# Optimization experiments

Hardware: AMD Instinct MI355X
Metric: run time of the kernel (lower is better)

Reference implementation:

```python
import jax, jax.numpy as jnp
import numpy as np

D_MODEL = 1024
NUM_HEADS = 16
HEAD_DIM = D_MODEL // NUM_HEADS


def setup_inputs() -> dict:
    key = jax.random.key(0)
    ks = jax.random.split(key, 5)
    scale = 1.0 / np.sqrt(D_MODEL)
    x = jax.random.normal(ks[0], (2, 2048, D_MODEL), dtype=jnp.float32)
    W_qkv = jax.random.normal(ks[1], (D_MODEL, 3 * D_MODEL), dtype=jnp.float32) * scale
    b_qkv = jnp.zeros((3 * D_MODEL,), dtype=jnp.float32)
    W_proj = jax.random.normal(ks[2], (D_MODEL, D_MODEL), dtype=jnp.float32) * scale
    b_proj = jnp.zeros((D_MODEL,), dtype=jnp.float32)
    return {"x": x, "W_qkv": W_qkv, "b_qkv": b_qkv, "W_proj": W_proj, "b_proj": b_proj}


def reference(x, W_qkv, b_qkv, W_proj, b_proj):
    B, S, D = x.shape
    qkv = x @ W_qkv + b_qkv                      # [B,S,3D]
    qkv = qkv.reshape(B, S, 3, NUM_HEADS, HEAD_DIM)
    qkv = jnp.transpose(qkv, (2, 0, 3, 1, 4))    # [3,B,H,S,hd]
    q, k, v = qkv[0], qkv[1], qkv[2]
    scores = jnp.einsum('bhqd,bhkd->bhqk', q, k) / jnp.sqrt(jnp.asarray(HEAD_DIM, x.dtype))
    probs = jax.nn.softmax(scores, axis=-1)
    out = jnp.einsum('bhqk,bhkd->bhqd', probs, v)  # [B,H,S,hd]
    out = jnp.transpose(out, (0, 2, 1, 3)).reshape(B, S, D)
    return out @ W_proj + b_proj
```

## Files before the change

### kernel.cpp

```cpp
#include <hip/hip_runtime.h>
#include <math.h>

#define B_ 2
#define S_ 2048
#define D_ 1024
#define H_ 16
#define HD_ 64

typedef __bf16 bf16x8 __attribute__((ext_vector_type(8)));
typedef __bf16 bf16x4 __attribute__((ext_vector_type(4)));
typedef __bf16 bf16x2 __attribute__((ext_vector_type(2)));
typedef float f32x4 __attribute__((ext_vector_type(4)));
typedef float f32x16 __attribute__((ext_vector_type(16)));
typedef unsigned u32x2 __attribute__((ext_vector_type(2)));

#define GLOAD16(gsrc, ldst) \
  __builtin_amdgcn_global_load_lds((const __attribute__((address_space(1))) void*)(gsrc), \
                                   (__attribute__((address_space(3))) void*)(ldst), 16, 0, 0)

#define QSCALE 0.18033688f

static __device__ __forceinline__ unsigned pack2(float a, float b) {
    bf16x2 v; v[0] = (__bf16)a; v[1] = (__bf16)b;
    return __builtin_bit_cast(unsigned, v);
}

__global__ __launch_bounds__(256) void prep_k(
    const float* __restrict__ x, __bf16* __restrict__ x_bf,
    const float* __restrict__ Wqkv, __bf16* __restrict__ wq_t,
    const float* __restrict__ Wproj, __bf16* __restrict__ wp_t)
{
    __shared__ float t[64][65];
    const int tid = threadIdx.x;
    const int bid = blockIdx.x;

    if (bid < 2048) {
        int i = (bid * 256 + tid) * 8;
        float4 a = *(const float4*)(x + i);
        float4 b = *(const float4*)(x + i + 4);
        bf16x8 v;
        v[0] = (__bf16)a.x; v[1] = (__bf16)a.y; v[2] = (__bf16)a.z; v[3] = (__bf16)a.w;
        v[4] = (__bf16)b.x; v[5] = (__bf16)b.y; v[6] = (__bf16)b.z; v[7] = (__bf16)b.w;
        *(bf16x8*)(x_bf + i) = v;
        return;
    }

    const float* in; __bf16* outp; int K, N, qcols; float qs; int bx, by;
    if (bid < 2816) {
        int tt = bid - 2048; bx = tt % 48; by = tt / 48;
        in = Wqkv; outp = wq_t; K = D_; N = 3 * D_; qcols = D_; qs = QSCALE;
    } else {
        int tt = bid - 2816; bx = tt % 16; by = tt / 16;
        in = Wproj; outp = wp_t; K = D_; N = D_; qcols = 0; qs = 1.0f;
    }
    const int bj = bx * 64;
    const int bi = by * 64;
    #pragma unroll
    for (int it = 0; it < 4; ++it) {
        int idx = (tid + it * 256) * 4;
        int r = idx >> 6, c = idx & 63;
        float4 v = *(const float4*)(in + (size_t)(bi + r) * N + bj + c);
        t[r][c] = v.x; t[r][c+1] = v.y; t[r][c+2] = v.z; t[r][c+3] = v.w;
    }
    __syncthreads();
    int j = tid & 63;
    int i0 = (tid >> 6) * 16;
    float s = (bj + j) < qcols ? qs : 1.0f;
    bf16x8 h0, h1;
    #pragma unroll
    for (int ii = 0; ii < 8; ++ii) h0[ii] = (__bf16)(t[i0 + ii][j] * s);
    #pragma unroll
    for (int ii = 0; ii < 8; ++ii) h1[ii] = (__bf16)(t[i0 + 8 + ii][j] * s);
    size_t o = (size_t)(bj + j) * K + bi + i0;
    *(bf16x8*)(outp + o) = h0; *(bf16x8*)(outp + o + 8) = h1;
}

template<typename OutT>
__global__ __launch_bounds__(256) void gemm_nt_k(
    const __bf16* __restrict__ A, const __bf16* __restrict__ Bt,
    const float* __restrict__ bias, OutT* __restrict__ C,
    int M, int N, int K, int qcols, float qs)
{
    constexpr int TSZ = 128 * 64;
    __shared__ __bf16 sA[TSZ];
    __shared__ __bf16 sB[TSZ];

    const int tid = threadIdx.x, w = tid >> 6, l = tid & 63;
    const int lr = l & 15, lg = l >> 4;
    const int bm = blockIdx.y * 128, bn = blockIdx.x * 128;
    const int wm = w >> 1, wn = w & 1;

    f32x4 acc[4][4] = {};

    for (int k0 = 0; k0 < K; k0 += 64) {
        __syncthreads();
        #pragma unroll
        for (int c = 0; c < 4; ++c) {
            int q = w * 4 + c;
            int r = q * 8 + (l >> 3);
            int sl = ((l & 7) ^ (r & 7)) * 8;
            GLOAD16(A + (size_t)(bm + r) * K + k0 + sl, sA + q * 512);
            GLOAD16(Bt + (size_t)(bn + r) * K + k0 + sl, sB + q * 512);
        }
        __syncthreads();
        #pragma unroll
        for (int kk = 0; kk < 2; ++kk) {
            bf16x8 ah[4], bh[4];
            #pragma unroll
            for (int i = 0; i < 4; ++i) {
                int ra = wm * 64 + i * 16 + lr;
                int sa = ((kk * 4 + lg) ^ (ra & 7)) * 8;
                ah[i] = *(const bf16x8*)(sA + ra * 64 + sa);
                int rb = wn * 64 + i * 16 + lr;
                int sb = ((kk * 4 + lg) ^ (rb & 7)) * 8;
                bh[i] = *(const bf16x8*)(sB + rb * 64 + sb);
            }
            #pragma unroll
            for (int mi = 0; mi < 4; ++mi)
                #pragma unroll
                for (int ni = 0; ni < 4; ++ni)
                    acc[mi][ni] = __builtin_amdgcn_mfma_f32_16x16x32_bf16(ah[mi], bh[ni], acc[mi][ni], 0, 0, 0);
        }
    }

    #pragma unroll
    for (int ni = 0; ni < 4; ++ni) {
        int col = bn + wn * 64 + ni * 16 + lr;
        float bv = bias[col];
        if (col < qcols) bv *= qs;
        #pragma unroll
        for (int mi = 0; mi < 4; ++mi) {
            #pragma unroll
            for (int r = 0; r < 4; ++r) {
                int row = bm + wm * 64 + mi * 16 + lg * 4 + r;
                float v = acc[mi][ni][r] + bv;
                C[(size_t)row * N + col] = (OutT)v;
            }
        }
    }
}

__global__ __launch_bounds__(256, 2) void attn32_k(
    const __bf16* __restrict__ qkv, __bf16* __restrict__ Pout,
    float* __restrict__ Lout)
{
    __shared__ __bf16 Ks[2][64 * 64];
    __shared__ __bf16 Vt[2][64 * 64];

    const int tid = threadIdx.x, w = tid >> 6, l = tid & 63;
    const int q32 = l & 31, hi = l >> 5;
    const int bid = blockIdx.x;
    const int X = bid >> 5, hb = bid & 31;
    const int qt = X >> 1, kvh = X & 1;
    const int h = hb >> 1, b = hb & 1;
    const int q0 = qt * 256;
    const int kvbase = kvh * 1024;
    const size_t ldq = 3 * D_;
    const __bf16* Qg = qkv + (size_t)b * S_ * ldq + h * HD_;
    const __bf16* Kg = Qg + D_;
    const __bf16* Vg = Qg + 2 * D_;
    const int qg0 = q0 + w * 64 + q32;

    bf16x8 qf0[4], qf1[4];
    #pragma unroll
    for (int ds = 0; ds < 4; ++ds) {
        qf0[ds] = *(const bf16x8*)(Qg + (size_t)qg0 * ldq + ds * 16 + hi * 8);
        qf1[ds] = *(const bf16x8*)(Qg + (size_t)(qg0 + 32) * ldq + ds * 16 + hi * 8);
    }

    int krow[2], ksl[2], voff[2][8];
    const int vk = l;
    #pragma unroll
    for (int c = 0; c < 2; ++c) {
        int p = (w * 2 + c) * 64 + l;
        krow[c] = p >> 3;
        ksl[c]  = (p & 7) ^ (krow[c] & 7);
        int d0 = (w * 2 + c) * 8;
        #pragma unroll
        for (int j = 0; j < 8; ++j)
            voff[c][j] = (d0 + j) * 128 + (((vk >> 3) ^ j) * 16) + (vk & 7) * 2;
    }

    f32x16 o0[2] = {}, o1[2] = {};
    float lsum0 = 0.f, lsum1 = 0.f;
    bf16x8 vr[2];

    auto stageK = [&](int lt, int buf) {
        #pragma unroll
        for (int c = 0; c < 2; ++c)
            GLOAD16(Kg + (size_t)(kvbase + lt * 64 + krow[c]) * ldq + ksl[c] * 8,
                    &Ks[buf][(w * 2 + c) * 512]);
    };
    auto loadV = [&](int lt) {
        #pragma unroll
        for (int c = 0; c < 2; ++c)
            vr[c] = *(const bf16x8*)(Vg + (size_t)(kvbase + lt * 64 + vk) * ldq + (w * 2 + c) * 8);
    };
    auto writeV = [&](int buf) {
        #pragma unroll
        for (int c = 0; c < 2; ++c)
            #pragma unroll
            for (int j = 0; j < 8; ++j)
                *(__bf16*)((char*)&Vt[buf][0] + voff[c][j]) = vr[c][j];
    };

    auto smPack = [&](f32x16 sc[2], bf16x8 pa[2][2], float& ls) {
        float sum = 0.f;
        #pragma unroll
        for (int kb = 0; kb < 2; ++kb)
            #pragma unroll
            for (int i = 0; i < 16; ++i) {
                float pv = __builtin_amdgcn_exp2f(sc[kb][i]);
                sc[kb][i] = pv;
                sum += pv;
            }
        ls += sum;
        #pragma unroll
        for (int kb = 0; kb < 2; ++kb)
            #pragma unroll
            for (int tl = 0; tl < 2; ++tl) {
                int base = tl * 8;
                unsigned A0 = pack2(sc[kb][base + 0], sc[kb][base + 1]);
                unsigned A1 = pack2(sc[kb][base + 2], sc[kb][base + 3]);
                unsigned B0 = pack2(sc[kb][base + 4], sc[kb][base + 5]);
                unsigned B1 = pack2(sc[kb][base + 6], sc[kb][base + 7]);
                u32x2 s0 = __builtin_amdgcn_permlane32_swap(A0, B0, false, false);
                u32x2 s1 = __builtin_amdgcn_permlane32_swap(A1, B1, false, false);
                union { unsigned u[4]; bf16x8 v; } pu;
                pu.u[0] = s0[0]; pu.u[1] = s1[0]; pu.u[2] = s0[1]; pu.u[3] = s1[1];
                pa[kb][tl] = pu.v;
            }
    };

    auto computeTile = [&](int cur) {
        f32x16 sc0[2] = {}, sc1[2] = {};
        __builtin_amdgcn_s_setprio(1);
        #pragma unroll
        for (int kb = 0; kb < 2; ++kb) {
            int r = kb * 32 + q32;
            #pragma unroll
            for (int ds = 0; ds < 4; ++ds) {
                int slot = (ds * 2 + hi) ^ (r & 7);
                bf16x8 kf = *(const bf16x8*)((const char*)&Ks[cur][0] + r * 128 + slot * 16);
                sc0[kb] = __builtin_amdgcn_mfma_f32_32x32x16_bf16(kf, qf0[ds], sc0[kb], 0, 0, 0);
                sc1[kb] = __builtin_amdgcn_mfma_f32_32x32x16_bf16(kf, qf1[ds], sc1[kb], 0, 0, 0);
            }
        }
        __builtin_amdgcn_s_setprio(0);

        bf16x8 pa0[2][2], pa1[2][2];
        smPack(sc0, pa0, lsum0);
        smPack(sc1, pa1, lsum1);

        __builtin_amdgcn_s_setprio(1);
        #pragma unroll
        for (int db = 0; db < 2; ++db) {
            int dr = db * 32 + q32;
            #pragma unroll
            for (int tt = 0; tt < 4; ++tt) {
                int slot = (tt * 2 + hi) ^ (dr & 7);
                bf16x8 vf = *(const bf16x8*)((const char*)&Vt[cur][0] + dr * 128 + slot * 16);
                o0[db] = __builtin_amdgcn_mfma_f32_32x32x16_bf16(vf, pa0[tt >> 1][tt & 1], o0[db], 0, 0, 0);
                o1[db] = __builtin_amdgcn_mfma_f32_32x32x16_bf16(vf, pa1[tt >> 1][tt & 1], o1[db], 0, 0, 0);
            }
        }
        __builtin_amdgcn_s_setprio(0);
    };

    stageK(0, 0);
    loadV(0);
    writeV(0);
    __syncthreads();

    constexpr int NT = 16;
    for (int kt = 0; kt < NT; ++kt) {
        const int cur = kt & 1, nxt = cur ^ 1;
        if (kt < NT - 1) { stageK(kt + 1, nxt); loadV(kt + 1); }
        computeTile(cur);
        if (kt < NT - 1) writeV(nxt);
        __syncthreads();
    }

    lsum0 += __shfl_xor(lsum0, 32);
    lsum1 += __shfl_xor(lsum1, 32);
    const size_t orow0 = (size_t)b * S_ + qg0;
    __bf16* Pb0 = Pout + (size_t)kvh * (4096 * 1024) + orow0 * D_ + h * HD_;
    __bf16* Pb1 = Pb0 + (size_t)32 * D_;
    #pragma unroll
    for (int db = 0; db < 2; ++db)
        #pragma unroll
        for (int rg = 0; rg < 4; ++rg) {
            int d = db * 32 + 8 * rg + 4 * hi;
            bf16x4 ov0, ov1;
            #pragma unroll
            for (int i = 0; i < 4; ++i) {
                ov0[i] = (__bf16)o0[db][rg * 4 + i];
                ov1[i] = (__bf16)o1[db][rg * 4 + i];
            }
            *(bf16x4*)(Pb0 + d) = ov0;
            *(bf16x4*)(Pb1 + d) = ov1;
        }
    if (hi == 0) {
        Lout[(size_t)kvh * (4096 * 16) + orow0 * 16 + h] = lsum0;
        Lout[(size_t)kvh * (4096 * 16) + (orow0 + 32) * 16 + h] = lsum1;
    }
}

__global__ __launch_bounds__(256) void combine_k(
    const __bf16* __restrict__ P, const float* __restrict__ L,
    __bf16* __restrict__ attnb)
{
    int i = (blockIdx.x * 256 + threadIdx.x) * 8;
    int row = i >> 10;
    int h = (i & 1023) >> 6;
    float l0 = L[row * 16 + h];
    float l1 = L[4096 * 16 + row * 16 + h];
    float inv = 1.0f / (l0 + l1);
    bf16x8 p0 = *(const bf16x8*)(P + i);
    bf16x8 p1 = *(const bf16x8*)(P + 4096 * 1024 + i);
    bf16x8 r;
    #pragma unroll
    for (int j = 0; j < 8; ++j)
        r[j] = (__bf16)(((float)p0[j] + (float)p1[j]) * inv);
    *(bf16x8*)(attnb + i) = r;
}

extern "C" void kernel_launch(void* const* d_in, const int* in_sizes, int n_in,
                              void* d_out, int out_size, void* d_ws, size_t ws_size,
                              hipStream_t stream) {
    const float* x     = (const float*)d_in[0];
    const float* Wqkv  = (const float*)d_in[1];
    const float* bqkv  = (const float*)d_in[2];
    const float* Wproj = (const float*)d_in[3];
    const float* bproj = (const float*)d_in[4];

    __bf16* ws = (__bf16*)d_ws;
    const size_t MB = 524288;
    __bf16* wp_t  = ws;
    __bf16* qkv   = ws + 2 * MB;
    __bf16* attnb = ws + 26 * MB;
    __bf16* x_bf  = ws + 34 * MB;
    __bf16* wq_t  = ws + 42 * MB;
    __bf16* Pp    = ws + 34 * MB;
    float*  Lp    = (float*)(ws + 50 * MB);

    const int M = B_ * S_;

    prep_k<<<3072, 256, 0, stream>>>(x, x_bf, Wqkv, wq_t, Wproj, wp_t);

    gemm_nt_k<__bf16><<<dim3(24, 32), 256, 0, stream>>>(
        x_bf, wq_t, bqkv, qkv, M, 3 * D_, D_, D_, QSCALE);

    attn32_k<<<512, 256, 0, stream>>>(qkv, Pp, Lp);

    combine_k<<<2048, 256, 0, stream>>>(Pp, Lp, attnb);

    gemm_nt_k<float><<<dim3(8, 32), 256, 0, stream>>>(
        attnb, wp_t, bproj, (float*)d_out, M, D_, D_, 0, 1.0f);
}
```

Before: 129.7 us.

## Replace QKV GEMM with 256x256 double-buffered 8-wave kernel and swizzle block order

The QKV projection now runs in a dedicated 512-thread kernel with 256x256 tiles. Loads for the next K slice are issued into a second LDS buffer while the current slice feeds the MFMAs, coordinated with explicit waitcnt/barrier and setprio. The kernel stages output through LDS so global stores are 16-byte and coalesced. Both GEMMs also remap block IDs in an XCD-aware swizzle to improve L2 locality. The cost is the full 128 KB of LDS, which allows one block per CU, plus fragile hand-written synchronization.

```diff
diff --git a/kernel.cpp b/kernel.cpp
--- a/kernel.cpp
+++ b/kernel.cpp
@@ -75,11 +75,109 @@
     *(bf16x8*)(outp + o) = h0; *(bf16x8*)(outp + o + 8) = h1;
 }
 
-template<typename OutT>
+__global__ __launch_bounds__(512) void gemm1_8ph_k(
+    const __bf16* __restrict__ A, const __bf16* __restrict__ Bt,
+    const float* __restrict__ bias, __bf16* __restrict__ C)
+{
+    constexpr int K = 1024, N = 3072, qcols = 1024;
+    __shared__ __bf16 smem[65536];
+
+    const int tid = threadIdx.x, w = tid >> 6, l = tid & 63;
+    const int lr = l & 15, lg = l >> 4;
+    const int wm = w >> 2, wn = w & 3;
+
+    const int bid = blockIdx.x;
+    const int swz = (bid & 7) * 24 + (bid >> 3);
+    const int bx = swz % 12, by = swz / 12;
+    const int bm = by * 256, bn = bx * 256;
+
+    const int rA = tid >> 2;
+    const int swcol = ((tid & 3) ^ (rA & 3)) * 8;
+    const size_t srcA0 = (size_t)(bm + rA) * K;
+    const size_t srcB0 = (size_t)(bn + rA) * K;
+
+    auto stage = [&](int k0, int s, int p) {
+        #pragma unroll
+        for (int h = 0; h < 2; ++h) {
+            GLOAD16(A + srcA0 + (size_t)h * 128 * K + k0 + p * 32 + swcol,
+                    smem + s * 16384 + p * 8192 + h * 4096 + w * 512);
+            GLOAD16(Bt + srcB0 + (size_t)h * 128 * K + k0 + p * 32 + swcol,
+                    smem + 32768 + s * 16384 + p * 8192 + h * 4096 + w * 512);
+        }
+    };
+
+    f32x4 acc[8][4] = {};
+
+    stage(0, 0, 0);
+    stage(0, 0, 1);
+    asm volatile("s_waitcnt vmcnt(4)" ::: "memory");
+    __builtin_amdgcn_s_barrier();
+
+    for (int kt = 0; kt < 16; ++kt) {
+        const int s = kt & 1;
+        #pragma unroll
+        for (int p = 0; p < 2; ++p) {
+            bf16x8 ah[8], bh[4];
+            const __bf16* baseA = smem + s * 16384 + p * 8192;
+            const __bf16* baseB = smem + 32768 + s * 16384 + p * 8192;
+            #pragma unroll
+            for (int j = 0; j < 4; ++j) {
+                int rb = wn * 64 + j * 16 + lr;
+                bh[j] = *(const bf16x8*)(baseB + rb * 32 + (lg ^ (rb & 3)) * 8);
+            }
+            #pragma unroll
+            for (int i = 0; i < 8; ++i) {
+                int ra = wm * 128 + i * 16 + lr;
+                ah[i] = *(const bf16x8*)(baseA + ra * 32 + (lg ^ (ra & 3)) * 8);
+            }
+            if (kt < 15) stage((kt + 1) * 64, s ^ 1, p);
+
+            __builtin_amdgcn_s_barrier();
+            asm volatile("s_waitcnt lgkmcnt(0)" ::: "memory");
+            __builtin_amdgcn_sched_barrier(0);
+            __builtin_amdgcn_s_setprio(1);
+            #pragma unroll
+            for (int i = 0; i < 8; ++i)
+                #pragma unroll
+                for (int j = 0; j < 4; ++j)
+                    acc[i][j] = __builtin_amdgcn_mfma_f32_16x16x32_bf16(ah[i], bh[j], acc[i][j], 0, 0, 0);
+            __builtin_amdgcn_s_setprio(0);
+
+            if (kt == 15 && p == 0)
+                asm volatile("s_waitcnt vmcnt(0)" ::: "memory");
+            else
+                asm volatile("s_waitcnt vmcnt(4)" ::: "memory");
+            __builtin_amdgcn_s_barrier();
+        }
+    }
+
+    __syncthreads();
+    #pragma unroll
+    for (int j = 0; j < 4; ++j) {
+        int col = wn * 64 + j * 16 + lr;
+        float bv = bias[bn + col];
+        if (bn + col < qcols) bv *= QSCALE;
+        #pragma unroll
+        for (int i = 0; i < 8; ++i)
+            #pragma unroll
+            for (int rr = 0; rr < 4; ++rr) {
+                int row = wm * 128 + i * 16 + lg * 4 + rr;
+                smem[row * 256 + col] = (__bf16)(acc[i][j][rr] + bv);
+            }
+    }
+    __syncthreads();
+    #pragma unroll
+    for (int pp = 0; pp < 16; ++pp) {
+        int idx = pp * 4096 + tid * 8;
+        int row = idx >> 8, col = idx & 255;
+        *(bf16x8*)(C + (size_t)(bm + row) * N + bn + col) = *(const bf16x8*)(smem + idx);
+    }
+}
+
 __global__ __launch_bounds__(256) void gemm_nt_k(
     const __bf16* __restrict__ A, const __bf16* __restrict__ Bt,
-    const float* __restrict__ bias, OutT* __restrict__ C,
-    int M, int N, int K, int qcols, float qs)
+    const float* __restrict__ bias, float* __restrict__ C,
+    int M, int N, int K)
 {
     constexpr int TSZ = 128 * 64;
     __shared__ __bf16 sA[TSZ];
@@ -87,7 +185,13 @@
 
     const int tid = threadIdx.x, w = tid >> 6, l = tid & 63;
     const int lr = l & 15, lg = l >> 4;
-    const int bm = blockIdx.y * 128, bn = blockIdx.x * 128;
+
+    const int nwg = gridDim.x;
+    const int bidl = blockIdx.x;
+    const int swz = (bidl & 7) * (nwg >> 3) + (bidl >> 3);
+    const int nbx = N >> 7;
+    const int bx = swz % nbx, by = swz / nbx;
+    const int bm = by * 128, bn = bx * 128;
     const int wm = w >> 1, wn = w & 1;
 
     f32x4 acc[4][4] = {};
@@ -127,14 +231,12 @@
     for (int ni = 0; ni < 4; ++ni) {
         int col = bn + wn * 64 + ni * 16 + lr;
         float bv = bias[col];
-        if (col < qcols) bv *= qs;
         #pragma unroll
         for (int mi = 0; mi < 4; ++mi) {
             #pragma unroll
             for (int r = 0; r < 4; ++r) {
                 int row = bm + wm * 64 + mi * 16 + lg * 4 + r;
-                float v = acc[mi][ni][r] + bv;
-                C[(size_t)row * N + col] = (OutT)v;
+                C[(size_t)row * N + col] = acc[mi][ni][r] + bv;
             }
         }
     }
@@ -344,17 +446,14 @@
     __bf16* Pp    = ws + 34 * MB;
     float*  Lp    = (float*)(ws + 50 * MB);
 
-    const int M = B_ * S_;
-
     prep_k<<<3072, 256, 0, stream>>>(x, x_bf, Wqkv, wq_t, Wproj, wp_t);
 
-    gemm_nt_k<__bf16><<<dim3(24, 32), 256, 0, stream>>>(
-        x_bf, wq_t, bqkv, qkv, M, 3 * D_, D_, D_, QSCALE);
+    gemm1_8ph_k<<<192, 512, 0, stream>>>(x_bf, wq_t, bqkv, qkv);
 
     attn32_k<<<512, 256, 0, stream>>>(qkv, Pp, Lp);
 
     combine_k<<<2048, 256, 0, stream>>>(Pp, Lp, attnb);
 
-    gemm_nt_k<float><<<dim3(8, 32), 256, 0, stream>>>(
-        attnb, wp_t, bproj, (float*)d_out, M, D_, D_, 0, 1.0f);
-}
+    gemm_nt_k<<<256, 256, 0, stream>>>(
+        attnb, wp_t, bproj, (float*)d_out, 4096, D_, D_);
+}
```

Measured after the change: 124.2 us. -4.3%, faster.
